# Kernel optimization log

Measured on AMD Instinct MI355X. Metric: run time of the kernel, lower is better.

## Reference

```python
import jax, jax.numpy as jnp
import numpy as np

B, T, D = 32, 512, 1024
EPS = 1e-12  # torch F.normalize eps


def smooth_l1(x):
    # nn.SmoothL1Loss default beta=1.0
    a = jnp.abs(x)
    return jnp.where(a < 1.0, 0.5 * x * x, a - 0.5)


def setup_inputs() -> dict:
    key = jax.random.key(0)
    k1, k2, k3, k4 = jax.random.split(key, 4)
    return {
        "word_targets": jax.random.normal(k1, (B, T, D), dtype=jnp.float32),
        "image_targets": jax.random.normal(k2, (B, D), dtype=jnp.float32),
        "preds": jax.random.normal(k3, (B, T, D), dtype=jnp.float32),
        "decode_lengths": jax.random.randint(k4, (B,), 1, T + 1, dtype=jnp.int32),
    }


def reference(word_targets, image_targets, preds, decode_lengths):
    # mask over valid (ragged) positions: [B, T]
    mask = (jnp.arange(T)[None, :] < decode_lengths[:, None]).astype(preds.dtype)
    lens = decode_lengths.astype(preds.dtype)  # [B]

    # word loss: per-sample mean of smooth_l1 over valid tokens x D
    sl1 = smooth_l1(preds - word_targets) * mask[:, :, None]  # [B,T,D]
    word_per_b = sl1.sum(axis=(1, 2)) / (lens * D)             # [B]
    word_loss = word_per_b.mean()

    # per-sentence means over valid tokens: [B, D]
    pred_mean = (preds * mask[:, :, None]).sum(axis=1) / lens[:, None]
    targ_mean = (word_targets * mask[:, :, None]).sum(axis=1) / lens[:, None]
    sentence_loss = smooth_l1(pred_mean - targ_mean).mean(axis=1).mean()

    # image embedding loss: compare pred sentence mean to L2-normalized image embedding
    norm = jnp.maximum(jnp.linalg.norm(image_targets, axis=-1, keepdims=True), EPS)
    img_norm = image_targets / norm
    image_loss = smooth_l1(pred_mean - img_norm).mean(axis=1).mean()

    return word_loss + sentence_loss + image_loss
```

## Files before the change

kernel.cpp:

```cpp
#include <hip/hip_runtime.h>
#include <math.h>

static constexpr int B_ = 32;
static constexpr int T_ = 512;
static constexpr int D_ = 1024;
static constexpr int WROWS_ = 64;
static constexpr int SLICE4_ = 32;
static constexpr int NSL_ = (D_ / 4) / SLICE4_;
static constexpr int GRID1_ = 1024;
static constexpr float EPS_ = 1e-12f;

__device__ __forceinline__ float sl1f(float x) {
    float a = fabsf(x);
    return a < 1.0f ? 0.5f * x * x : a - 0.5f;
}

__device__ __forceinline__ float blockReduce256(float v, float* lds) {
#pragma unroll
    for (int o = 32; o > 0; o >>= 1) v += __shfl_down(v, o, 64);
    int wid = threadIdx.x >> 6, lane = threadIdx.x & 63;
    if (lane == 0) lds[wid] = v;
    __syncthreads();
    float tot = lds[0] + lds[1] + lds[2] + lds[3];
    __syncthreads();
    return tot;
}

__global__ __launch_bounds__(256, 4) void pass1_kernel(
    const float* __restrict__ preds, const float* __restrict__ wtarg,
    const int* __restrict__ lens,
    float* __restrict__ wsPred, float* __restrict__ wsTarg,
    float* __restrict__ wsSl1, float* __restrict__ out)
{
    __shared__ float4 redP[8][SLICE4_];
    __shared__ float4 redT[8][SLICE4_];
    __shared__ float lred[4];
    __shared__ int sEx[B_ + 1];
    __shared__ int sNwin[B_];
    __shared__ int sLen[B_];

    const int tid = threadIdx.x;
    if (blockIdx.x == 0 && tid == 0) out[0] = 0.f;

    if (tid < 64) {
        int len_t = (tid < B_) ? lens[tid] : 0;
        int nwin = (len_t + WROWS_ - 1) / WROWS_;
        int nu = nwin * NSL_;
        int incl = nu;
#pragma unroll
        for (int o = 1; o < 64; o <<= 1) {
            int u = __shfl_up(incl, o, 64);
            if (tid >= o) incl += u;
        }
        if (tid < B_) { sEx[tid] = incl - nu; sNwin[tid] = nwin; sLen[tid] = len_t; }
        if (tid == B_ - 1) sEx[B_] = incl;
    }
    __syncthreads();
    const int total = sEx[B_];

    const int j = tid & (SLICE4_ - 1);
    const int r8 = tid >> 5;

    for (int fu = blockIdx.x; fu < total; fu += GRID1_) {
        int lo = 0, hi = B_;
        while (hi - lo > 1) {
            int mid = (lo + hi) >> 1;
            if (sEx[mid] <= fu) lo = mid; else hi = mid;
        }
        const int b = lo;
        const int rem = fu - sEx[b];
        const int nwin = sNwin[b];
        const int s = rem / nwin;
        const int w = rem - s * nwin;
        const int len = sLen[b];
        const int t0 = w * WROWS_;
        const int nr = min(WROWS_, len - t0);

        const float4* pp = reinterpret_cast<const float4*>(preds)
                           + (size_t)(b * T_ + t0) * (D_ / 4) + s * SLICE4_ + j;
        const float4* pw = reinterpret_cast<const float4*>(wtarg)
                           + (size_t)(b * T_ + t0) * (D_ / 4) + s * SLICE4_ + j;

        float4 ps = make_float4(0.f, 0.f, 0.f, 0.f);
        float4 ts = make_float4(0.f, 0.f, 0.f, 0.f);
        float sl = 0.f;

        if (nr == WROWS_) {
            float4 p[8], wv[8];
#pragma unroll
            for (int k = 0; k < 8; ++k) p[k] = pp[(size_t)(r8 + 8 * k) * (D_ / 4)];
#pragma unroll
            for (int k = 0; k < 8; ++k) wv[k] = pw[(size_t)(r8 + 8 * k) * (D_ / 4)];
#pragma unroll
            for (int k = 0; k < 8; ++k) {
                ps.x += p[k].x; ps.y += p[k].y; ps.z += p[k].z; ps.w += p[k].w;
                ts.x += wv[k].x; ts.y += wv[k].y; ts.z += wv[k].z; ts.w += wv[k].w;
                sl += sl1f(p[k].x - wv[k].x) + sl1f(p[k].y - wv[k].y)
                    + sl1f(p[k].z - wv[k].z) + sl1f(p[k].w - wv[k].w);
            }
        } else {
            for (int k = 0; k < 8; ++k) {
                int r = r8 + 8 * k;
                if (r < nr) {
                    float4 p = pp[(size_t)r * (D_ / 4)];
                    float4 wv = pw[(size_t)r * (D_ / 4)];
                    ps.x += p.x; ps.y += p.y; ps.z += p.z; ps.w += p.w;
                    ts.x += wv.x; ts.y += wv.y; ts.z += wv.z; ts.w += wv.w;
                    sl += sl1f(p.x - wv.x) + sl1f(p.y - wv.y)
                        + sl1f(p.z - wv.z) + sl1f(p.w - wv.w);
                }
            }
        }

        redP[r8][j] = ps;
        redT[r8][j] = ts;
        float tot = blockReduce256(sl, lred);

        if (tid < SLICE4_) {
            float4 ap = make_float4(0.f, 0.f, 0.f, 0.f);
            float4 at = make_float4(0.f, 0.f, 0.f, 0.f);
#pragma unroll
            for (int k = 0; k < 8; ++k) {
                float4 a = redP[k][tid], bb = redT[k][tid];
                ap.x += a.x; ap.y += a.y; ap.z += a.z; ap.w += a.w;
                at.x += bb.x; at.y += bb.y; at.z += bb.z; at.w += bb.w;
            }
            const size_t off = (size_t)fu * SLICE4_ + tid;
            reinterpret_cast<float4*>(wsPred)[off] = ap;
            reinterpret_cast<float4*>(wsTarg)[off] = at;
        }
        if (tid == 0) wsSl1[fu] = tot;
        __syncthreads();
    }
}

__global__ __launch_bounds__(256) void pass2_kernel(
    const float* __restrict__ img, const int* __restrict__ lens,
    const float* __restrict__ wsPred, const float* __restrict__ wsTarg,
    const float* __restrict__ wsSl1, float* __restrict__ out)
{
    __shared__ float lred[4];
    __shared__ int sEx[B_ + 1];
    __shared__ int sNwin[B_];

    const int b = blockIdx.x, tid = threadIdx.x;
    if (tid < 64) {
        int len_t = (tid < B_) ? lens[tid] : 0;
        int nwin = (len_t + WROWS_ - 1) / WROWS_;
        int nu = nwin * NSL_;
        int incl = nu;
#pragma unroll
        for (int o = 1; o < 64; o <<= 1) {
            int u = __shfl_up(incl, o, 64);
            if (tid >= o) incl += u;
        }
        if (tid < B_) { sEx[tid] = incl - nu; sNwin[tid] = nwin; }
        if (tid == B_ - 1) sEx[B_] = incl;
    }
    __syncthreads();

    const int base = sEx[b];
    const int nwin = sNwin[b];
    const int len = lens[b];
    const float flen = (float)len;
    const int s = tid >> 5, col = tid & 31;

    float4 ps = make_float4(0.f, 0.f, 0.f, 0.f);
    float4 ts = make_float4(0.f, 0.f, 0.f, 0.f);
    for (int w = 0; w < nwin; ++w) {
        const size_t off = (size_t)(base + s * nwin + w) * SLICE4_ + col;
        float4 p = reinterpret_cast<const float4*>(wsPred)[off];
        float4 t = reinterpret_cast<const float4*>(wsTarg)[off];
        ps.x += p.x; ps.y += p.y; ps.z += p.z; ps.w += p.w;
        ts.x += t.x; ts.y += t.y; ts.z += t.z; ts.w += t.w;
    }

    const float4* img4 = reinterpret_cast<const float4*>(img);
    float4 im = img4[(size_t)b * (D_ / 4) + tid];
    float ss = im.x * im.x + im.y * im.y + im.z * im.z + im.w * im.w;
    float sumsq = blockReduce256(ss, lred);
    float inv_norm = 1.0f / fmaxf(sqrtf(sumsq), EPS_);

    const float pmx = ps.x / flen, pmy = ps.y / flen, pmz = ps.z / flen, pmw = ps.w / flen;
    const float tmx = ts.x / flen, tmy = ts.y / flen, tmz = ts.z / flen, tmw = ts.w / flen;

    float sv = sl1f(pmx - tmx) + sl1f(pmy - tmy) + sl1f(pmz - tmz) + sl1f(pmw - tmw)
             + sl1f(pmx - im.x * inv_norm) + sl1f(pmy - im.y * inv_norm)
             + sl1f(pmz - im.z * inv_norm) + sl1f(pmw - im.w * inv_norm);
    float tot = blockReduce256(sv, lred);

    float wv = (tid < nwin * NSL_) ? wsSl1[base + tid] : 0.f;
    if (tid < 64) {
#pragma unroll
        for (int o = 32; o > 0; o >>= 1) wv += __shfl_down(wv, o, 64);
    }

    if (tid == 0) {
        float per_b = tot / (float)D_ + wv / (flen * (float)D_);
        atomicAdd(out, per_b * (1.0f / (float)B_));
    }
}

extern "C" void kernel_launch(void* const* d_in, const int* in_sizes, int n_in,
                              void* d_out, int out_size, void* d_ws, size_t ws_size,
                              hipStream_t stream) {
    const float* wtarg = (const float*)d_in[0];
    const float* img   = (const float*)d_in[1];
    const float* preds = (const float*)d_in[2];
    const int*   lens  = (const int*)d_in[3];
    float* out = (float*)d_out;

    float* wsPred = (float*)d_ws;
    float* wsTarg = wsPred + (size_t)2048 * 128;
    float* wsSl1  = wsTarg + (size_t)2048 * 128;

    pass1_kernel<<<GRID1_, 256, 0, stream>>>(preds, wtarg, lens,
                                             wsPred, wsTarg, wsSl1, out);
    pass2_kernel<<<B_, 256, 0, stream>>>(img, lens, wsPred, wsTarg, wsSl1, out);
}
```

Measured before the change: 25.91 us.

## Fuse finalize pass into main kernel via per-sample last-block counters

```diff
diff --git a/kernel.cpp b/kernel.cpp
--- a/kernel.cpp
+++ b/kernel.cpp
@@ -26,11 +26,32 @@
     return tot;
 }
 
-__global__ __launch_bounds__(256, 4) void pass1_kernel(
+__device__ __forceinline__ void store_f4_sc(float4* dst, float4 v) {
+    unsigned long long* p = reinterpret_cast<unsigned long long*>(dst);
+    union { float2 f; unsigned long long u; } lo, hi;
+    lo.f = make_float2(v.x, v.y); hi.f = make_float2(v.z, v.w);
+    __hip_atomic_store(p, lo.u, __ATOMIC_RELAXED, __HIP_MEMORY_SCOPE_SYSTEM);
+    __hip_atomic_store(p + 1, hi.u, __ATOMIC_RELAXED, __HIP_MEMORY_SCOPE_SYSTEM);
+}
+__device__ __forceinline__ float4 load_f4_sc(const float4* src) {
+    const unsigned long long* p = reinterpret_cast<const unsigned long long*>(src);
+    unsigned long long a = __hip_atomic_load(p, __ATOMIC_RELAXED, __HIP_MEMORY_SCOPE_SYSTEM);
+    unsigned long long b = __hip_atomic_load(p + 1, __ATOMIC_RELAXED, __HIP_MEMORY_SCOPE_SYSTEM);
+    union { unsigned long long u; float2 f; } ua, ub;
+    ua.u = a; ub.u = b;
+    return make_float4(ua.f.x, ua.f.y, ub.f.x, ub.f.y);
+}
+
+__global__ __launch_bounds__(64) void init_kernel(int* __restrict__ ctrs) {
+    if (threadIdx.x < B_ + 1) ctrs[threadIdx.x] = 0;
+}
+
+__global__ __launch_bounds__(256, 4) void main_kernel(
     const float* __restrict__ preds, const float* __restrict__ wtarg,
-    const int* __restrict__ lens,
+    const float* __restrict__ img, const int* __restrict__ lens,
     float* __restrict__ wsPred, float* __restrict__ wsTarg,
-    float* __restrict__ wsSl1, float* __restrict__ out)
+    float* __restrict__ wsSl1, float* __restrict__ wsPerB,
+    int* __restrict__ ctrs, float* __restrict__ out)
 {
     __shared__ float4 redP[8][SLICE4_];
     __shared__ float4 redT[8][SLICE4_];
@@ -38,9 +59,10 @@
     __shared__ int sEx[B_ + 1];
     __shared__ int sNwin[B_];
     __shared__ int sLen[B_];
+    __shared__ int sFinB;
+    __shared__ int sFin2;
 
     const int tid = threadIdx.x;
-    if (blockIdx.x == 0 && tid == 0) out[0] = 0.f;
 
     if (tid < 64) {
         int len_t = (tid < B_) ? lens[tid] : 0;
@@ -60,6 +82,7 @@
 
     const int j = tid & (SLICE4_ - 1);
     const int r8 = tid >> 5;
+    const float4* img4 = reinterpret_cast<const float4*>(img);
 
     for (int fu = blockIdx.x; fu < total; fu += GRID1_) {
         int lo = 0, hi = B_;
@@ -126,78 +149,79 @@
                 at.x += bb.x; at.y += bb.y; at.z += bb.z; at.w += bb.w;
             }
             const size_t off = (size_t)fu * SLICE4_ + tid;
-            reinterpret_cast<float4*>(wsPred)[off] = ap;
-            reinterpret_cast<float4*>(wsTarg)[off] = at;
-        }
-        if (tid == 0) wsSl1[fu] = tot;
+            store_f4_sc(reinterpret_cast<float4*>(wsPred) + off, ap);
+            store_f4_sc(reinterpret_cast<float4*>(wsTarg) + off, at);
+        }
+        if (tid == 0) {
+            __hip_atomic_store(&wsSl1[fu], tot, __ATOMIC_RELAXED, __HIP_MEMORY_SCOPE_SYSTEM);
+            asm volatile("s_waitcnt vmcnt(0)" ::: "memory");
+            int old = atomicAdd(&ctrs[b], 1);
+            sFinB = (old == nwin * NSL_ - 1) ? b : -1;
+        }
         __syncthreads();
-    }
-}
-
-__global__ __launch_bounds__(256) void pass2_kernel(
-    const float* __restrict__ img, const int* __restrict__ lens,
-    const float* __restrict__ wsPred, const float* __restrict__ wsTarg,
-    const float* __restrict__ wsSl1, float* __restrict__ out)
-{
-    __shared__ float lred[4];
-    __shared__ int sEx[B_ + 1];
-    __shared__ int sNwin[B_];
-
-    const int b = blockIdx.x, tid = threadIdx.x;
-    if (tid < 64) {
-        int len_t = (tid < B_) ? lens[tid] : 0;
-        int nwin = (len_t + WROWS_ - 1) / WROWS_;
-        int nu = nwin * NSL_;
-        int incl = nu;
-#pragma unroll
-        for (int o = 1; o < 64; o <<= 1) {
-            int u = __shfl_up(incl, o, 64);
-            if (tid >= o) incl += u;
-        }
-        if (tid < B_) { sEx[tid] = incl - nu; sNwin[tid] = nwin; }
-        if (tid == B_ - 1) sEx[B_] = incl;
-    }
-    __syncthreads();
-
-    const int base = sEx[b];
-    const int nwin = sNwin[b];
-    const int len = lens[b];
-    const float flen = (float)len;
-    const int s = tid >> 5, col = tid & 31;
-
-    float4 ps = make_float4(0.f, 0.f, 0.f, 0.f);
-    float4 ts = make_float4(0.f, 0.f, 0.f, 0.f);
-    for (int w = 0; w < nwin; ++w) {
-        const size_t off = (size_t)(base + s * nwin + w) * SLICE4_ + col;
-        float4 p = reinterpret_cast<const float4*>(wsPred)[off];
-        float4 t = reinterpret_cast<const float4*>(wsTarg)[off];
-        ps.x += p.x; ps.y += p.y; ps.z += p.z; ps.w += p.w;
-        ts.x += t.x; ts.y += t.y; ts.z += t.z; ts.w += t.w;
-    }
-
-    const float4* img4 = reinterpret_cast<const float4*>(img);
-    float4 im = img4[(size_t)b * (D_ / 4) + tid];
-    float ss = im.x * im.x + im.y * im.y + im.z * im.z + im.w * im.w;
-    float sumsq = blockReduce256(ss, lred);
-    float inv_norm = 1.0f / fmaxf(sqrtf(sumsq), EPS_);
-
-    const float pmx = ps.x / flen, pmy = ps.y / flen, pmz = ps.z / flen, pmw = ps.w / flen;
-    const float tmx = ts.x / flen, tmy = ts.y / flen, tmz = ts.z / flen, tmw = ts.w / flen;
-
-    float sv = sl1f(pmx - tmx) + sl1f(pmy - tmy) + sl1f(pmz - tmz) + sl1f(pmw - tmw)
-             + sl1f(pmx - im.x * inv_norm) + sl1f(pmy - im.y * inv_norm)
-             + sl1f(pmz - im.z * inv_norm) + sl1f(pmw - im.w * inv_norm);
-    float tot = blockReduce256(sv, lred);
-
-    float wv = (tid < nwin * NSL_) ? wsSl1[base + tid] : 0.f;
-    if (tid < 64) {
-#pragma unroll
-        for (int o = 32; o > 0; o >>= 1) wv += __shfl_down(wv, o, 64);
-    }
-
-    if (tid == 0) {
-        float per_b = tot / (float)D_ + wv / (flen * (float)D_);
-        atomicAdd(out, per_b * (1.0f / (float)B_));
+        const int fb = sFinB;
+
+        if (fb >= 0) {
+            const int fnwin = sNwin[fb];
+            const int fbase = sEx[fb];
+            const float flen = (float)sLen[fb];
+            const int fs = tid >> 5, fcol = tid & 31;
+
+            float4 aps = make_float4(0.f, 0.f, 0.f, 0.f);
+            float4 ats = make_float4(0.f, 0.f, 0.f, 0.f);
+            for (int ww = 0; ww < fnwin; ++ww) {
+                const size_t off = (size_t)(fbase + fs * fnwin + ww) * SLICE4_ + fcol;
+                float4 p = load_f4_sc(reinterpret_cast<const float4*>(wsPred) + off);
+                float4 t = load_f4_sc(reinterpret_cast<const float4*>(wsTarg) + off);
+                aps.x += p.x; aps.y += p.y; aps.z += p.z; aps.w += p.w;
+                ats.x += t.x; ats.y += t.y; ats.z += t.z; ats.w += t.w;
+            }
+
+            float4 im = img4[(size_t)fb * (D_ / 4) + tid];
+            float ss = im.x * im.x + im.y * im.y + im.z * im.z + im.w * im.w;
+            float sumsq = blockReduce256(ss, lred);
+            float inv_norm = 1.0f / fmaxf(sqrtf(sumsq), EPS_);
+
+            const float pmx = aps.x / flen, pmy = aps.y / flen, pmz = aps.z / flen, pmw = aps.w / flen;
+            const float tmx = ats.x / flen, tmy = ats.y / flen, tmz = ats.z / flen, tmw = ats.w / flen;
+
+            float sv = sl1f(pmx - tmx) + sl1f(pmy - tmy) + sl1f(pmz - tmz) + sl1f(pmw - tmw)
+                     + sl1f(pmx - im.x * inv_norm) + sl1f(pmy - im.y * inv_norm)
+                     + sl1f(pmz - im.z * inv_norm) + sl1f(pmw - im.w * inv_norm);
+            float stot = blockReduce256(sv, lred);
+
+            float wv = 0.f;
+            if (tid < fnwin * NSL_)
+                wv = __hip_atomic_load(&wsSl1[fbase + tid], __ATOMIC_RELAXED,
+                                       __HIP_MEMORY_SCOPE_SYSTEM);
+            if (tid < 64) {
+#pragma unroll
+                for (int o = 32; o > 0; o >>= 1) wv += __shfl_down(wv, o, 64);
+            }
+
+            if (tid == 0) {
+                float per_b = stot / (float)D_ + wv / (flen * (float)D_);
+                __hip_atomic_store(&wsPerB[fb], per_b, __ATOMIC_RELAXED,
+                                   __HIP_MEMORY_SCOPE_SYSTEM);
+                asm volatile("s_waitcnt vmcnt(0)" ::: "memory");
+                int old2 = atomicAdd(&ctrs[B_], 1);
+                sFin2 = (old2 == B_ - 1) ? 1 : 0;
+            }
+            __syncthreads();
+
+            if (sFin2) {
+                float v = 0.f;
+                if (tid < B_)
+                    v = __hip_atomic_load(&wsPerB[tid], __ATOMIC_RELAXED,
+                                          __HIP_MEMORY_SCOPE_SYSTEM);
+                if (tid < 64) {
+#pragma unroll
+                    for (int o = 32; o > 0; o >>= 1) v += __shfl_down(v, o, 64);
+                }
+                if (tid == 0) out[0] = v / (float)B_;
+            }
+        }
+        __syncthreads();
     }
 }
 
@@ -213,8 +237,10 @@
     float* wsPred = (float*)d_ws;
     float* wsTarg = wsPred + (size_t)2048 * 128;
     float* wsSl1  = wsTarg + (size_t)2048 * 128;
-
-    pass1_kernel<<<GRID1_, 256, 0, stream>>>(preds, wtarg, lens,
-                                             wsPred, wsTarg, wsSl1, out);
-    pass2_kernel<<<B_, 256, 0, stream>>>(img, lens, wsPred, wsTarg, wsSl1, out);
-}
+    float* wsPerB = wsSl1 + 2048;
+    int*   ctrs   = (int*)(wsPerB + B_);
+
+    init_kernel<<<1, 64, 0, stream>>>(ctrs);
+    main_kernel<<<GRID1_, 256, 0, stream>>>(preds, wtarg, img, lens,
+                                            wsPred, wsTarg, wsSl1, wsPerB, ctrs, out);
+}
```

New measurement: 38.75 us. 49.5% more time.
